# Performance work log

Hardware: AMD Instinct MI355X
Metric: run time of the kernel (lower is better)

The kernel has to match this reference:

```python
import jax, jax.numpy as jnp
import numpy as np

DIM = 512
NUM_HEADS = 8
DIM_HEAD = 64
INNER = NUM_HEADS * DIM_HEAD  # 512
EPS = 1e-5


def setup_inputs() -> dict:
    key = jax.random.key(0)
    ks = jax.random.split(key, 6)
    B, H, W = 16, 64, 64
    x = jax.random.normal(ks[0], (B, DIM, H, W), dtype=jnp.float32)
    # 1x1 conv weights stored as [out, in]
    w_qkv = jax.random.normal(ks[1], (3 * INNER, DIM), dtype=jnp.float32) * (1.0 / np.sqrt(DIM))
    w_out = jax.random.normal(ks[2], (DIM, INNER), dtype=jnp.float32) * (1.0 / np.sqrt(INNER))
    b_out = jax.random.normal(ks[3], (DIM,), dtype=jnp.float32) * 0.01
    gamma = jnp.ones((DIM,), dtype=jnp.float32)
    beta = jnp.zeros((DIM,), dtype=jnp.float32)
    return {"x": x, "w_qkv": w_qkv, "w_out": w_out, "b_out": b_out,
            "gamma": gamma, "beta": beta}


def reference(x, w_qkv, w_out, b_out, gamma, beta):
    B, C, H, W = x.shape
    N = H * W
    # 1x1 conv == channel GEMM
    qkv = jnp.einsum('bchw,oc->bohw', x, w_qkv)            # [B, 3*INNER, H, W]
    qkv = qkv.reshape(B, 3, NUM_HEADS, DIM_HEAD, N)        # chunk along channel
    q, k, v = qkv[:, 0], qkv[:, 1], qkv[:, 2]              # each [B, h, Dh, N]
    # NOTE: faithful to source — attention over channel dim (Dh x Dh), not N x N
    scores = jnp.einsum('bhdn,bhen->bhde', q, k) / np.sqrt(DIM_HEAD)
    attn = jax.nn.softmax(scores, axis=-1)                 # [B, h, Dh, Dh]
    out = jnp.einsum('bhde,bhen->bhdn', attn, v)           # [B, h, Dh, N]
    out = out.reshape(B, INNER, H, W)
    out = jnp.einsum('bchw,oc->bohw', out, w_out) + b_out[None, :, None, None]
    # GroupNorm with 1 group == per-sample layernorm over (C,H,W) with channel affine
    mean = jnp.mean(out, axis=(1, 2, 3), keepdims=True)
    var = jnp.var(out, axis=(1, 2, 3), keepdims=True)
    out = (out - mean) * jax.lax.rsqrt(var + EPS)
    out = out * gamma[None, :, None, None] + beta[None, :, None, None]
    return out
```

## Files before the change

kernel.cpp:

```cpp
#include <hip/hip_runtime.h>

typedef __bf16 bf16;
typedef __bf16 bf16x8 __attribute__((ext_vector_type(8)));
typedef __bf16 bf16x4 __attribute__((ext_vector_type(4)));
typedef float  f32x4  __attribute__((ext_vector_type(4)));

#define BATCH   16
#define CDIM    512
#define NSPAT   4096
#define QKV_M   1536
#define INNER   512
#define GK      512

__device__ __forceinline__ void gld16(const bf16* g, const bf16* l) {
  __builtin_amdgcn_global_load_lds(
      (const __attribute__((address_space(1))) void*)g,
      (__attribute__((address_space(3))) void*)l, 16, 0, 0);
}

#define SBAR() do { asm volatile("" ::: "memory"); __builtin_amdgcn_s_barrier(); \
                    asm volatile("" ::: "memory"); } while (0)
#define VMCNT(n) asm volatile("s_waitcnt vmcnt(" #n ")" ::: "memory")

__global__ __launch_bounds__(256) void cast_f32_bf16_kernel(
    const float* __restrict__ in, bf16* __restrict__ out, int n4) {
  int i = blockIdx.x * 256 + threadIdx.x;
  if (i >= n4) return;
  float4 v = ((const float4*)in)[i];
  bf16x4 o = { (bf16)v.x, (bf16)v.y, (bf16)v.z, (bf16)v.w };
  *(bf16x4*)(out + (size_t)i * 4) = o;
}

__global__ __launch_bounds__(256) void transpose_cast_kernel(
    const float* __restrict__ x, bf16* __restrict__ xt) {
  __shared__ __attribute__((aligned(16))) bf16 T[64][72];
  int b = blockIdx.z, c0 = blockIdx.y * 64, n0 = blockIdx.x * 64;
  int t = threadIdx.x;
  const float* xp = x + ((size_t)b * CDIM + c0) * NSPAT + n0;
#pragma unroll
  for (int i = 0; i < 4; ++i) {
    int v = t + i * 256;
    int c = v >> 4, nq = (v & 15) * 4;
    float4 rd = *(const float4*)(xp + (size_t)c * NSPAT + nq);
    T[nq + 0][c] = (bf16)rd.x; T[nq + 1][c] = (bf16)rd.y;
    T[nq + 2][c] = (bf16)rd.z; T[nq + 3][c] = (bf16)rd.w;
  }
  __syncthreads();
  bf16* op = xt + ((size_t)b * NSPAT + n0) * CDIM + c0;
#pragma unroll
  for (int i = 0; i < 2; ++i) {
    int v = t + i * 256;
    int n = v >> 3, cc = (v & 7) * 8;
    *(bf16x8*)(op + (size_t)n * CDIM + cc) = *(const bf16x8*)&T[n][cc];
  }
}

template <int OUTMODE>
__global__ __launch_bounds__(512, 2) void gemm256_kernel(
    const bf16* __restrict__ A, const bf16* __restrict__ Bt,
    void* __restrict__ Cout, const float* __restrict__ bias,
    float* __restrict__ part, int M, int N) {
  __shared__ __attribute__((aligned(16))) bf16 Sm[65536];

  int bz = blockIdx.z;
  int m0 = blockIdx.y * 256, n0 = blockIdx.x * 256;
  int tid = threadIdx.x, lane = tid & 63, wid = tid >> 6;
  int wm = wid >> 2, wn = wid & 3;
  int lm = lane & 15, kqd = lane >> 4;

  int aoff[8], boff[4];
#pragma unroll
  for (int mf = 0; mf < 8; ++mf) {
    int x = (mf * 16 + lm) * 4 + kqd;
    aoff[mf] = wm * 4096 + (x ^ ((x >> 3) & 7)) * 8;
  }
#pragma unroll
  for (int nf = 0; nf < 4; ++nf) {
    int x = ((wn & 1) * 64 + nf * 16 + lm) * 4 + kqd;
    boff[nf] = 8192 + (wn >> 1) * 4096 + (x ^ ((x >> 3) & 7)) * 8;
  }

  int sl = tid ^ ((tid >> 3) & 7);
  int srow = sl >> 2, sc8 = (sl & 3) * 8;
  const bf16* aS = A + (size_t)(m0 + srow) * GK + sc8;
  const bf16* bS = Bt + ((size_t)bz * N + n0 + srow) * GK + sc8;

  f32x4 acc[8][4] = {};

#define STG_A(t) do { bf16* d = Sm + (((t)) & 3) * 16384 + wid * 512; \
    gld16(aS + (size_t)(t) * 32, d); \
    gld16(aS + (size_t)128 * GK + (size_t)(t) * 32, d + 4096); } while (0)
#define STG_B(t) do { bf16* d = Sm + (((t)) & 3) * 16384 + 8192 + wid * 512; \
    gld16(bS + (size_t)(t) * 32, d); \
    gld16(bS + (size_t)128 * GK + (size_t)(t) * 32, d + 4096); } while (0)

  STG_A(0); STG_B(0); STG_A(1); STG_B(1); STG_A(2); STG_B(2);
  VMCNT(8);
  SBAR();

#define TILE_BODY(t, DOSTG, WAITK) do { \
    const bf16* Sb = Sm + ((t) & 3) * 16384; \
    bf16x8 af[8], bq[4]; \
    _Pragma("unroll") for (int i = 0; i < 4; ++i) af[i] = *(const bf16x8*)(Sb + aoff[i]); \
    _Pragma("unroll") for (int i = 0; i < 4; ++i) bq[i] = *(const bf16x8*)(Sb + boff[i]); \
    _Pragma("unroll") for (int i = 0; i < 4; ++i) af[4 + i] = *(const bf16x8*)(Sb + aoff[4 + i]); \
    if (DOSTG) { STG_A((t) + 3); STG_B((t) + 3); } \
    __builtin_amdgcn_s_setprio(1); \
    _Pragma("unroll") for (int i = 0; i < 4; ++i) \
      _Pragma("unroll") for (int j = 0; j < 4; ++j) \
        acc[i][j] = __builtin_amdgcn_mfma_f32_16x16x32_bf16(af[i], bq[j], acc[i][j], 0, 0, 0); \
    _Pragma("unroll") for (int i = 0; i < 4; ++i) \
      _Pragma("unroll") for (int j = 0; j < 4; ++j) \
        acc[4 + i][j] = __builtin_amdgcn_mfma_f32_16x16x32_bf16(af[4 + i], bq[j], acc[4 + i][j], 0, 0, 0); \
    __builtin_amdgcn_s_setprio(0); \
    WAITK; \
    SBAR(); \
  } while (0)

  for (int tt = 0; tt < 12; tt += 4) {
#pragma unroll
    for (int q = 0; q < 4; ++q) TILE_BODY(tt + q, 1, VMCNT(8));
  }
  TILE_BODY(12, 1, VMCNT(8));
  TILE_BODY(13, 0, VMCNT(4));
  TILE_BODY(14, 0, VMCNT(0));
  TILE_BODY(15, 0, (void)0);

  if (OUTMODE == 0) {
    bf16* C = (bf16*)Cout + (size_t)bz * M * N;
    bf16* Ws = Sm + wid * 8192;
#pragma unroll
    for (int mf = 0; mf < 8; ++mf)
#pragma unroll
      for (int nf = 0; nf < 4; ++nf)
#pragma unroll
        for (int r = 0; r < 4; ++r)
          Ws[(mf * 16 + kqd * 4 + r) * 64 + nf * 16 + lm] = (bf16)acc[mf][nf][r];
#pragma unroll
    for (int j = 0; j < 16; ++j) {
      int u = j * 64 + lane;
      int row = u >> 3, cu = (u & 7) * 8;
      *(bf16x8*)(C + (size_t)(m0 + wm * 128 + row) * N + (n0 + wn * 64 + cu)) =
          *(const bf16x8*)&Ws[row * 64 + cu];
    }
  } else {
    float* C = (float*)Cout + (size_t)bz * M * N;
    float s = 0.f, s2 = 0.f;
#pragma unroll
    for (int mf = 0; mf < 8; ++mf)
#pragma unroll
      for (int nf = 0; nf < 4; ++nf) {
        int row = m0 + wm * 128 + mf * 16 + kqd * 4;
        int col = n0 + wn * 64 + nf * 16 + lm;
#pragma unroll
        for (int r = 0; r < 4; ++r) {
          float v = acc[mf][nf][r] + bias[row + r];
          C[(size_t)(row + r) * N + col] = v;
          s += v; s2 += v * v;
        }
      }
#pragma unroll
    for (int off = 32; off > 0; off >>= 1) {
      s  += __shfl_down(s, off, 64);
      s2 += __shfl_down(s2, off, 64);
    }
    if (lane == 0) {
      atomicAdd(&part[bz * 2],     s);
      atomicAdd(&part[bz * 2 + 1], s2);
    }
  }
#undef TILE_BODY
#undef STG_A
#undef STG_B
}

template <int OUTMODE>
__global__ __launch_bounds__(256) void gemm_tn_kernel(
    const bf16* __restrict__ A, const bf16* __restrict__ Bt,
    void* __restrict__ Cout, const float* __restrict__ bias,
    float* __restrict__ part, int M, int N, int K) {
  __shared__ __attribute__((aligned(16))) bf16 smem[8192];

  int b  = blockIdx.z;
  int m0 = blockIdx.y * 128, n0 = blockIdx.x * 128;
  const bf16* Ab = A + (size_t)m0 * K;
  const bf16* Bb = Bt + ((size_t)b * N + n0) * K;

  int tid = threadIdx.x, lane = tid & 63, wid = tid >> 6;
  int wm = wid >> 1, wn = wid & 1, lm = lane & 15, kqd = lane >> 4;
  int srow = lane >> 2, skb = lane & 3;

  f32x4 acc[4][4] = {};

  for (int k0 = 0; k0 < K; k0 += 32) {
#pragma unroll
    for (int i = 0; i < 2; ++i) {
      int gi = wid * 2 + i;
      gld16(Ab + (size_t)(gi * 16 + srow) * K + k0 + skb * 8, smem + gi * 512);
      gld16(Bb + (size_t)(gi * 16 + srow) * K + k0 + skb * 8, smem + 4096 + gi * 512);
    }
    __syncthreads();
    bf16x8 af[4], bfr[4];
#pragma unroll
    for (int im = 0; im < 4; ++im)
      af[im] = *(const bf16x8*)&smem[(wm * 64 + im * 16 + lm) * 32 + kqd * 8];
#pragma unroll
    for (int in = 0; in < 4; ++in)
      bfr[in] = *(const bf16x8*)&smem[4096 + (wn * 64 + in * 16 + lm) * 32 + kqd * 8];
#pragma unroll
    for (int im = 0; im < 4; ++im)
#pragma unroll
      for (int in = 0; in < 4; ++in)
        acc[im][in] = __builtin_amdgcn_mfma_f32_16x16x32_bf16(af[im], bfr[in], acc[im][in], 0, 0, 0);
    __syncthreads();
  }

  if (OUTMODE == 0) {
    bf16* C = (bf16*)Cout + (size_t)b * M * N;
    bf16* Ws = smem + wid * 2048;
#pragma unroll
    for (int half = 0; half < 2; ++half) {
#pragma unroll
      for (int im2 = 0; im2 < 2; ++im2) {
        int im = half * 2 + im2;
#pragma unroll
        for (int in = 0; in < 4; ++in)
#pragma unroll
          for (int r = 0; r < 4; ++r)
            Ws[(im2 * 16 + kqd * 4 + r) * 64 + in * 16 + lm] = (bf16)acc[im][in][r];
      }
#pragma unroll
      for (int j = 0; j < 4; ++j) {
        int u = lane + j * 64;
        int row = u >> 3, cu = (u & 7) * 8;
        *(bf16x8*)(C + (size_t)(m0 + wm * 64 + half * 32 + row) * N + n0 + wn * 64 + cu) =
            *(const bf16x8*)&Ws[row * 64 + cu];
      }
    }
  } else {
    float* C = (float*)Cout + (size_t)b * M * N;
    float s = 0.f, s2 = 0.f;
#pragma unroll
    for (int im = 0; im < 4; ++im)
#pragma unroll
      for (int in = 0; in < 4; ++in) {
        int row = m0 + wm * 64 + im * 16 + kqd * 4;
        int col = n0 + wn * 64 + in * 16 + lm;
#pragma unroll
        for (int r = 0; r < 4; ++r) {
          float v = acc[im][in][r] + bias[row + r];
          C[(size_t)(row + r) * N + col] = v;
          s += v; s2 += v * v;
        }
      }
#pragma unroll
    for (int off = 32; off > 0; off >>= 1) {
      s  += __shfl_down(s, off, 64);
      s2 += __shfl_down(s2, off, 64);
    }
    __shared__ float red[8];
    if (lane == 0) { red[wid] = s; red[wid + 4] = s2; }
    __syncthreads();
    if (tid == 0) {
      atomicAdd(&part[b * 2],     red[0] + red[1] + red[2] + red[3]);
      atomicAdd(&part[b * 2 + 1], red[4] + red[5] + red[6] + red[7]);
    }
  }
}

__global__ __launch_bounds__(256) void attn_scores_kernel(
    const bf16* __restrict__ qkv, float* __restrict__ sc_part) {
  __shared__ __attribute__((aligned(16))) bf16 qs[4096];
  int chunk = blockIdx.x, bh = blockIdx.y, b = bh >> 3, h = bh & 7;
  const bf16* q = qkv + ((size_t)b * QKV_M + h * 64) * NSPAT + chunk * 512;
  const bf16* k = q + (size_t)INNER * NSPAT;

  int tid = threadIdx.x, lane = tid & 63, wid = tid >> 6;
  int lm = lane & 15, kqd = lane >> 4, d0 = wid * 16;
  int srow = lane >> 2, skb = lane & 3;

  f32x4 acc[4] = {};
  for (int n0 = 0; n0 < 512; n0 += 32) {
    gld16(q + (size_t)(wid * 16 + srow) * NSPAT + n0 + skb * 8, qs + wid * 512);
    gld16(k + (size_t)(wid * 16 + srow) * NSPAT + n0 + skb * 8, qs + 2048 + wid * 512);
    __syncthreads();
    bf16x8 a = *(const bf16x8*)&qs[(d0 + lm) * 32 + kqd * 8];
#pragma unroll
    for (int eb = 0; eb < 4; ++eb) {
      bf16x8 bb = *(const bf16x8*)&qs[2048 + (eb * 16 + lm) * 32 + kqd * 8];
      acc[eb] = __builtin_amdgcn_mfma_f32_16x16x32_bf16(a, bb, acc[eb], 0, 0, 0);
    }
    __syncthreads();
  }
  float* outp = sc_part + ((size_t)bh * 8 + chunk) * 4096;
#pragma unroll
  for (int eb = 0; eb < 4; ++eb)
#pragma unroll
    for (int r = 0; r < 4; ++r)
      outp[(d0 + kqd * 4 + r) * 64 + eb * 16 + lm] = acc[eb][r];
}

__global__ __launch_bounds__(256) void attn_softmax_kernel(
    const float* __restrict__ sc_part, bf16* __restrict__ attn_w) {
  __shared__ float ssum[64][65];
  int bh = blockIdx.x, t = threadIdx.x;
  const float* p = sc_part + (size_t)bh * 8 * 4096;
  float v[16];
#pragma unroll
  for (int j = 0; j < 16; ++j) v[j] = p[t + j * 256];
  for (int c = 1; c < 8; ++c)
#pragma unroll
    for (int j = 0; j < 16; ++j) v[j] += p[c * 4096 + t + j * 256];
#pragma unroll
  for (int j = 0; j < 16; ++j) {
    int q = t + j * 256;
    ssum[q >> 6][q & 63] = v[j];
  }
  __syncthreads();
  if (t < 64) {
    float mx = -1e30f;
    for (int e = 0; e < 64; ++e) mx = fmaxf(mx, ssum[t][e]);
    float s = 0.f;
    for (int e = 0; e < 64; ++e) {
      float ex = __expf((ssum[t][e] - mx) * 0.125f);
      ssum[t][e] = ex; s += ex;
    }
    float inv = 1.0f / s;
    bf16* ow = attn_w + (size_t)bh * 4096 + t * 64;
    for (int e = 0; e < 64; ++e) ow[e] = (bf16)(ssum[t][e] * inv);
  }
}

__global__ __launch_bounds__(256) void attn_pv_kernel(
    const bf16* __restrict__ qkv, const bf16* __restrict__ attn_w,
    bf16* __restrict__ attn_t) {
  __shared__ __attribute__((aligned(16))) bf16 aw[64 * 72];
  __shared__ __attribute__((aligned(16))) bf16 Vs[128 * 72];
  int chunk = blockIdx.x, bh = blockIdx.y, b = bh >> 3, h = bh & 7;
  const bf16* vmat = qkv + ((size_t)b * QKV_M + 2 * INNER + h * 64) * NSPAT + chunk * 512;
  bf16* outt = attn_t + ((size_t)b * NSPAT + chunk * 512) * INNER + h * 64;

  int tid = threadIdx.x, lane = tid & 63, wid = tid >> 6;
  int lm = lane & 15, kqd = lane >> 4, d0 = wid * 16;

#pragma unroll
  for (int i = 0; i < 2; ++i) {
    int v = tid + i * 256;
    *(bf16x8*)&aw[(v >> 3) * 72 + (v & 7) * 8] = *(const bf16x8*)(attn_w + (size_t)bh * 4096 + v * 8);
  }
  __syncthreads();
  bf16x8 a0 = *(const bf16x8*)&aw[(d0 + lm) * 72 + kqd * 8];
  bf16x8 a1 = *(const bf16x8*)&aw[(d0 + lm) * 72 + 32 + kqd * 8];

  for (int nc = 0; nc < 512; nc += 128) {
    __syncthreads();
#pragma unroll
    for (int i = 0; i < 4; ++i) {
      int v = i * 256 + tid;
      int e = v & 63, nn = (v >> 6) * 8;
      bf16x8 d = *(const bf16x8*)(vmat + (size_t)e * NSPAT + nc + nn);
#pragma unroll
      for (int j = 0; j < 8; ++j) Vs[(nn + j) * 72 + e] = d[j];
    }
    __syncthreads();
    f32x4 o[8];
#pragma unroll
    for (int nt = 0; nt < 8; ++nt) {
      bf16x8 b0 = *(const bf16x8*)&Vs[(nt * 16 + lm) * 72 + kqd * 8];
      bf16x8 b1 = *(const bf16x8*)&Vs[(nt * 16 + lm) * 72 + 32 + kqd * 8];
      o[nt] = (f32x4){0.f, 0.f, 0.f, 0.f};
      o[nt] = __builtin_amdgcn_mfma_f32_16x16x32_bf16(a0, b0, o[nt], 0, 0, 0);
      o[nt] = __builtin_amdgcn_mfma_f32_16x16x32_bf16(a1, b1, o[nt], 0, 0, 0);
    }
    __syncthreads();
#pragma unroll
    for (int nt = 0; nt < 8; ++nt) {
      bf16x4 ov = { (bf16)o[nt][0], (bf16)o[nt][1], (bf16)o[nt][2], (bf16)o[nt][3] };
      *(bf16x4*)&Vs[(nt * 16 + lm) * 72 + d0 + kqd * 4] = ov;
    }
    __syncthreads();
#pragma unroll
    for (int i = 0; i < 4; ++i) {
      int v = i * 256 + tid;
      int n = v >> 3, dc = (v & 7) * 8;
      *(bf16x8*)(outt + (size_t)(nc + n) * INNER + dc) = *(const bf16x8*)&Vs[n * 72 + dc];
    }
  }
}

__global__ void ln_stats_kernel(const float* __restrict__ part, float2* __restrict__ stats) {
  int b = threadIdx.x;
  if (b < 16) {
    const float invn = 1.0f / 2097152.0f;
    float mean = part[b * 2] * invn;
    float var  = part[b * 2 + 1] * invn - mean * mean;
    stats[b] = make_float2(mean, rsqrtf(var + 1e-5f));
  }
}

__global__ __launch_bounds__(256) void ln_apply_kernel(
    float* __restrict__ out, const float2* __restrict__ stats,
    const float* __restrict__ gamma, const float* __restrict__ beta) {
  size_t i4 = (size_t)blockIdx.x * 256 + threadIdx.x;
  size_t e  = i4 * 4;
  int b = (int)(e >> 21);
  int c = (int)((e >> 12) & 511);
  float2 st = stats[b];
  float g  = gamma[c] * st.y;
  float bb = beta[c] - st.x * g;
  float4* p = (float4*)out;
  float4 v = p[i4];
  v.x = v.x * g + bb; v.y = v.y * g + bb; v.z = v.z * g + bb; v.w = v.w * g + bb;
  p[i4] = v;
}

extern "C" void kernel_launch(void* const* d_in, const int* in_sizes, int n_in,
                              void* d_out, int out_size, void* d_ws, size_t ws_size,
                              hipStream_t stream) {
  const float* x      = (const float*)d_in[0];
  const float* w_qkv  = (const float*)d_in[1];
  const float* w_out  = (const float*)d_in[2];
  const float* b_out  = (const float*)d_in[3];
  const float* gamma  = (const float*)d_in[4];
  const float* beta   = (const float*)d_in[5];
  float* out = (float*)d_out;

  char* ws = (char*)d_ws;
  bf16*   xt      = (bf16*)(ws);
  float*  sc_part = (float*)(ws);
  bf16*   attn_w  = (bf16*)(ws + 16777216);
  bf16*   wqkvb   = (bf16*)(ws + 67108864);
  bf16*   woutb   = (bf16*)(ws + 68681728);
  bf16*   qkvb    = (bf16*)(ws + 69206016);
  bf16*   attn_t  = (bf16*)(ws + 270532608);
  float*  part    = (float*)(ws + 337641472);
  float2* stats   = (float2*)(ws + 337641600);

  hipMemsetAsync(part, 0, 128, stream);

  transpose_cast_kernel<<<dim3(64, 8, BATCH), 256, 0, stream>>>(x, xt);
  cast_f32_bf16_kernel<<<768, 256, 0, stream>>>(w_qkv, wqkvb, 196608);
  cast_f32_bf16_kernel<<<256, 256, 0, stream>>>(w_out, woutb, 65536);

  gemm256_kernel<0><<<dim3(16, 6, BATCH), 512, 0, stream>>>(
      wqkvb, xt, (void*)qkvb, nullptr, nullptr, QKV_M, NSPAT);

  attn_scores_kernel<<<dim3(8, 128), 256, 0, stream>>>(qkvb, sc_part);
  attn_softmax_kernel<<<128, 256, 0, stream>>>(sc_part, attn_w);
  attn_pv_kernel<<<dim3(8, 128), 256, 0, stream>>>(qkvb, attn_w, attn_t);

  gemm_tn_kernel<1><<<dim3(32, 4, BATCH), 256, 0, stream>>>(
      woutb, attn_t, (void*)out, b_out, part, INNER, NSPAT, CDIM);

  ln_stats_kernel<<<1, 16, 0, stream>>>(part, stats);
  ln_apply_kernel<<<32768, 256, 0, stream>>>(out, stats, gamma, beta);
}
```

Before: 546.3 us.

## Double-buffer LDS fragment reads in registers to overlap with MFMA

Restructures the GEMM main loop so the LDS fragments for the next K-tile are read into a second register set while MFMAs run on the current set. The loop is unrolled by two with ping-pong register buffers, and the vmcnt waits are retuned to match. The aim is to hide LDS read latency behind matrix-core work, at the cost of about 48 extra VGPRs per thread, which may lower occupancy or cause spills.

Result: slower. 594.9 us (+8.9%).

```diff
diff --git a/kernel.cpp b/kernel.cpp
--- a/kernel.cpp
+++ b/kernel.cpp
@@ -86,6 +86,7 @@
   const bf16* bS = Bt + ((size_t)bz * N + n0 + srow) * GK + sc8;
 
   f32x4 acc[8][4] = {};
+  bf16x8 afA[8], bqA[4], afB[8], bqB[4];
 
 #define STG_A(t) do { bf16* d = Sm + (((t)) & 3) * 16384 + wid * 512; \
     gld16(aS + (size_t)(t) * 32, d); \
@@ -94,37 +95,46 @@
     gld16(bS + (size_t)(t) * 32, d); \
     gld16(bS + (size_t)128 * GK + (size_t)(t) * 32, d + 4096); } while (0)
 
-  STG_A(0); STG_B(0); STG_A(1); STG_B(1); STG_A(2); STG_B(2);
-  VMCNT(8);
-  SBAR();
-
-#define TILE_BODY(t, DOSTG, WAITK) do { \
-    const bf16* Sb = Sm + ((t) & 3) * 16384; \
-    bf16x8 af[8], bq[4]; \
-    _Pragma("unroll") for (int i = 0; i < 4; ++i) af[i] = *(const bf16x8*)(Sb + aoff[i]); \
+#define RD(af, bq, slot) do { \
+    const bf16* Sb = Sm + (slot) * 16384; \
+    _Pragma("unroll") for (int i = 0; i < 8; ++i) af[i] = *(const bf16x8*)(Sb + aoff[i]); \
     _Pragma("unroll") for (int i = 0; i < 4; ++i) bq[i] = *(const bf16x8*)(Sb + boff[i]); \
-    _Pragma("unroll") for (int i = 0; i < 4; ++i) af[4 + i] = *(const bf16x8*)(Sb + aoff[4 + i]); \
-    if (DOSTG) { STG_A((t) + 3); STG_B((t) + 3); } \
+  } while (0)
+
+#define MM(af, bq) do { \
     __builtin_amdgcn_s_setprio(1); \
-    _Pragma("unroll") for (int i = 0; i < 4; ++i) \
+    _Pragma("unroll") for (int i = 0; i < 8; ++i) \
       _Pragma("unroll") for (int j = 0; j < 4; ++j) \
         acc[i][j] = __builtin_amdgcn_mfma_f32_16x16x32_bf16(af[i], bq[j], acc[i][j], 0, 0, 0); \
-    _Pragma("unroll") for (int i = 0; i < 4; ++i) \
-      _Pragma("unroll") for (int j = 0; j < 4; ++j) \
-        acc[4 + i][j] = __builtin_amdgcn_mfma_f32_16x16x32_bf16(af[4 + i], bq[j], acc[4 + i][j], 0, 0, 0); \
     __builtin_amdgcn_s_setprio(0); \
-    WAITK; \
-    SBAR(); \
   } while (0)
 
-  for (int tt = 0; tt < 12; tt += 4) {
-#pragma unroll
-    for (int q = 0; q < 4; ++q) TILE_BODY(tt + q, 1, VMCNT(8));
-  }
-  TILE_BODY(12, 1, VMCNT(8));
-  TILE_BODY(13, 0, VMCNT(4));
-  TILE_BODY(14, 0, VMCNT(0));
-  TILE_BODY(15, 0, (void)0);
+  STG_A(0); STG_B(0); STG_A(1); STG_B(1); STG_A(2); STG_B(2);
+  VMCNT(4);
+  SBAR();
+  RD(afA, bqA, 0);
+
+  for (int tt = 0; tt < 12; tt += 2) {
+    STG_A(tt + 3); STG_B(tt + 3);
+    RD(afB, bqB, (tt + 1) & 3);
+    MM(afA, bqA);
+    VMCNT(4); SBAR();
+    STG_A(tt + 4); STG_B(tt + 4);
+    RD(afA, bqA, (tt + 2) & 3);
+    MM(afB, bqB);
+    VMCNT(4); SBAR();
+  }
+  STG_A(15); STG_B(15);
+  RD(afB, bqB, 13 & 3);
+  MM(afA, bqA);
+  VMCNT(4); SBAR();
+  RD(afA, bqA, 14 & 3);
+  MM(afB, bqB);
+  VMCNT(0); SBAR();
+  RD(afB, bqB, 15 & 3);
+  MM(afA, bqA);
+  MM(afB, bqB);
+  SBAR();
 
   if (OUTMODE == 0) {
     bf16* C = (bf16*)Cout + (size_t)bz * M * N;
@@ -169,7 +179,8 @@
       atomicAdd(&part[bz * 2 + 1], s2);
     }
   }
-#undef TILE_BODY
+#undef MM
+#undef RD
 #undef STG_A
 #undef STG_B
 }
```

## Software-pipeline LDS fragment reads across k-tiles with double-buffered registers

Applied to the files above, without the earlier changes.

Restructures the GEMM main loop so that the A and B fragments for the next k-tile are read from LDS while the second half of the current tile's MFMAs runs. Register buffers are double-buffered and alternate between iterations, and each tile is split into two MFMA halves separated by a barrier. The goal is to hide LDS read latency behind matrix math. In exchange it adds a second barrier per tile and raises register pressure, which could lower occupancy or cause spills.

After: 563.5 us. 1.03x slower.

```diff
diff --git a/kernel.cpp b/kernel.cpp
--- a/kernel.cpp
+++ b/kernel.cpp
@@ -86,6 +86,7 @@
   const bf16* bS = Bt + ((size_t)bz * N + n0 + srow) * GK + sc8;
 
   f32x4 acc[8][4] = {};
+  bf16x8 h1[4], h0A[4], h0B[4], bqA[4], bqB[4];
 
 #define STG_A(t) do { bf16* d = Sm + (((t)) & 3) * 16384 + wid * 512; \
     gld16(aS + (size_t)(t) * 32, d); \
@@ -94,37 +95,53 @@
     gld16(bS + (size_t)(t) * 32, d); \
     gld16(bS + (size_t)128 * GK + (size_t)(t) * 32, d + 4096); } while (0)
 
+#define RDA(dst, slot, half) do { \
+    const bf16* Sb = Sm + (slot) * 16384; \
+    _Pragma("unroll") for (int i = 0; i < 4; ++i) \
+      dst[i] = *(const bf16x8*)(Sb + aoff[(half) * 4 + i]); \
+  } while (0)
+#define RDB(dst, slot) do { \
+    const bf16* Sb = Sm + (slot) * 16384; \
+    _Pragma("unroll") for (int i = 0; i < 4; ++i) \
+      dst[i] = *(const bf16x8*)(Sb + boff[i]); \
+  } while (0)
+
+#define MMH(hbase, af, bq) do { \
+    __builtin_amdgcn_s_setprio(1); \
+    _Pragma("unroll") for (int i = 0; i < 4; ++i) \
+      _Pragma("unroll") for (int j = 0; j < 4; ++j) \
+        acc[(hbase) + i][j] = __builtin_amdgcn_mfma_f32_16x16x32_bf16(af[i], bq[j], acc[(hbase) + i][j], 0, 0, 0); \
+    __builtin_amdgcn_s_setprio(0); \
+  } while (0)
+
+#define BODY(t, C0, CB, N0, NB, DOSTG, WAITM) do { \
+    RDA(h1, (t) & 3, 1); \
+    if (DOSTG) { STG_A((t) + 3); STG_B((t) + 3); } \
+    MMH(0, C0, CB); \
+    WAITM; \
+    SBAR(); \
+    RDA(N0, ((t) + 1) & 3, 0); \
+    RDB(NB, ((t) + 1) & 3); \
+    MMH(4, h1, CB); \
+    SBAR(); \
+  } while (0)
+
   STG_A(0); STG_B(0); STG_A(1); STG_B(1); STG_A(2); STG_B(2);
   VMCNT(8);
   SBAR();
-
-#define TILE_BODY(t, DOSTG, WAITK) do { \
-    const bf16* Sb = Sm + ((t) & 3) * 16384; \
-    bf16x8 af[8], bq[4]; \
-    _Pragma("unroll") for (int i = 0; i < 4; ++i) af[i] = *(const bf16x8*)(Sb + aoff[i]); \
-    _Pragma("unroll") for (int i = 0; i < 4; ++i) bq[i] = *(const bf16x8*)(Sb + boff[i]); \
-    _Pragma("unroll") for (int i = 0; i < 4; ++i) af[4 + i] = *(const bf16x8*)(Sb + aoff[4 + i]); \
-    if (DOSTG) { STG_A((t) + 3); STG_B((t) + 3); } \
-    __builtin_amdgcn_s_setprio(1); \
-    _Pragma("unroll") for (int i = 0; i < 4; ++i) \
-      _Pragma("unroll") for (int j = 0; j < 4; ++j) \
-        acc[i][j] = __builtin_amdgcn_mfma_f32_16x16x32_bf16(af[i], bq[j], acc[i][j], 0, 0, 0); \
-    _Pragma("unroll") for (int i = 0; i < 4; ++i) \
-      _Pragma("unroll") for (int j = 0; j < 4; ++j) \
-        acc[4 + i][j] = __builtin_amdgcn_mfma_f32_16x16x32_bf16(af[4 + i], bq[j], acc[4 + i][j], 0, 0, 0); \
-    __builtin_amdgcn_s_setprio(0); \
-    WAITK; \
-    SBAR(); \
-  } while (0)
-
-  for (int tt = 0; tt < 12; tt += 4) {
-#pragma unroll
-    for (int q = 0; q < 4; ++q) TILE_BODY(tt + q, 1, VMCNT(8));
-  }
-  TILE_BODY(12, 1, VMCNT(8));
-  TILE_BODY(13, 0, VMCNT(4));
-  TILE_BODY(14, 0, VMCNT(0));
-  TILE_BODY(15, 0, (void)0);
+  RDB(bqA, 0); RDA(h0A, 0, 0);
+
+  for (int tt = 0; tt < 12; tt += 2) {
+    BODY(tt,     h0A, bqA, h0B, bqB, 1, VMCNT(8));
+    BODY(tt + 1, h0B, bqB, h0A, bqA, 1, VMCNT(8));
+  }
+  BODY(12, h0A, bqA, h0B, bqB, 1, VMCNT(8));
+  BODY(13, h0B, bqB, h0A, bqA, 0, VMCNT(4));
+  BODY(14, h0A, bqA, h0B, bqB, 0, VMCNT(0));
+  RDA(h1, 3, 1);
+  MMH(0, h0B, bqB);
+  MMH(4, h1, bqB);
+  SBAR();
 
   if (OUTMODE == 0) {
     bf16* C = (bf16*)Cout + (size_t)bz * M * N;
@@ -169,7 +186,10 @@
       atomicAdd(&part[bz * 2 + 1], s2);
     }
   }
-#undef TILE_BODY
+#undef BODY
+#undef MMH
+#undef RDA
+#undef RDB
 #undef STG_A
 #undef STG_B
 }
```
